# Optimization experiments

Hardware: AMD Instinct MI355X
Metric: run time of the kernel (lower is better)

## Reference

```python
import jax, jax.numpy as jnp
import numpy as np

B = 4096        # batch size (graphs)
NPB = 64        # nodes per graph
G = 8           # max_groups; first G nodes of each graph are group super-nodes
D = 128         # node_dim
GD = 128        # global_dim
H = 64          # hidden_dim
NEG = jnp.float32(-1e9)


def setup_inputs() -> dict:
    key = jax.random.key(0)
    k = jax.random.split(key, 5)
    node_features = jax.random.normal(k[0], (B * NPB, D), dtype=jnp.float32)
    global_features = jax.random.normal(k[1], (B, GD), dtype=jnp.float32)
    # nodes sorted by graph: graph b owns rows [b*NPB, (b+1)*NPB)
    batch = jnp.repeat(jnp.arange(B, dtype=jnp.int64), NPB)
    local_id = jnp.tile(jnp.arange(NPB), B)
    group_mask_nodes = local_id < G            # exactly G group nodes per graph, in order
    dock_mask = jax.random.bernoulli(k[2], 0.7, (B, G, G))
    W1 = jax.random.normal(k[3], (GD + 2 * D, H), dtype=jnp.float32) * 0.05
    b1 = jnp.zeros((H,), dtype=jnp.float32)
    W2 = jax.random.normal(k[4], (H, 1), dtype=jnp.float32) * 0.05
    b2 = jnp.zeros((1,), dtype=jnp.float32)
    return {
        "node_features": node_features,
        "global_features": global_features,
        "group_mask_nodes": group_mask_nodes,
        "batch": batch,
        "dock_mask": dock_mask,
        "W1": W1, "b1": b1, "W2": W2, "b2": b2,
    }


def reference(node_features, global_features, group_mask_nodes, batch, dock_mask, W1, b1, W2, b2):
    bsz = global_features.shape[0]
    g = dock_mask.shape[1]
    d = node_features.shape[-1]
    # Gather group super-nodes. Rows are sorted by graph with exactly g group
    # nodes per graph, so a static-size nonzero reshapes to [B, G, D] preserving
    # the row order the torch loop relies on.
    idx = jnp.nonzero(group_mask_nodes, size=bsz * g)[0]
    group_nodes = node_features[idx].reshape(bsz, g, d)           # [B,G,D]
    # Build all (i,j) pair features: [global_b, g_i, g_j] -> [B,G,G,GD+2D]
    glob = jnp.broadcast_to(global_features[:, None, None, :], (bsz, g, g, global_features.shape[-1]))
    gi = jnp.broadcast_to(group_nodes[:, :, None, :], (bsz, g, g, d))
    gj = jnp.broadcast_to(group_nodes[:, None, :, :], (bsz, g, g, d))
    inp = jnp.concatenate([glob, gi, gj], axis=-1)
    # Tiny 2-layer MLP scorer, fully batched over all pairs.
    h = jax.nn.relu(jnp.einsum('bijf,fh->bijh', inp, W1) + b1)
    scores = jnp.einsum('bijh,ho->bijo', h, W2)[..., 0] + b2[0]   # [B,G,G]
    offdiag = ~jnp.eye(g, dtype=bool)
    logits = jnp.where(offdiag[None, :, :], scores, NEG)
    logits = jnp.where(dock_mask, logits, NEG)
    return logits.reshape(bsz, g * g)
```

## Files before the change

kernel.cpp:

```cpp
#include <hip/hip_runtime.h>
#include <hip/hip_bf16.h>

#define NEGV (-1e9f)

typedef __attribute__((ext_vector_type(8))) short short8;
typedef __attribute__((ext_vector_type(4))) float f32x4;

#define MFMA16(a, b, c) __builtin_amdgcn_mfma_f32_16x16x32_bf16(a, b, c, 0, 0, 0)

__device__ __forceinline__ unsigned short f2bf(float x) {
    union { __hip_bfloat16 h; unsigned short u; } c;
    c.h = __float2bfloat16(x);
    return c.u;
}

__device__ __forceinline__ short8 pack2(f32x4 a, f32x4 b) {
    short8 r;
    r[0] = (short)f2bf(a[0]); r[1] = (short)f2bf(a[1]);
    r[2] = (short)f2bf(a[2]); r[3] = (short)f2bf(a[3]);
    r[4] = (short)f2bf(b[0]); r[5] = (short)f2bf(b[1]);
    r[6] = (short)f2bf(b[2]); r[7] = (short)f2bf(b[3]);
    return r;
}

__device__ __forceinline__ short8 pack8(const float* v) {
    short8 r;
#pragma unroll
    for (int i = 0; i < 8; ++i) r[i] = (short)f2bf(v[i]);
    return r;
}

__global__ __launch_bounds__(256, 4) void dock_main(
    const float* __restrict__ nodes,
    const float* __restrict__ glob,
    const int*   __restrict__ dock,
    const float* __restrict__ W1,
    const float* __restrict__ b1,
    const float* __restrict__ W2,
    const float* __restrict__ b2,
    float* __restrict__ out)
{
    __shared__ __align__(16) unsigned char smem[18048];
    unsigned char* gA  = smem;
    unsigned char* gGl = smem + 8192;
    float* sPQ = (float*)smem;
    float* sA  = (float*)(smem + 16896);

    const int t    = threadIdx.x;
    const int lane = t & 63;
    const int w    = __builtin_amdgcn_readfirstlane(t >> 6);
    const int b0   = blockIdx.x * 4;
    const int lr   = lane & 15, lg = lane >> 4;

    short8 bq0f[4], bq1f[4], bgf[4];
    {
        const int n0 = w * 32 + lr;
        const int n1 = n0 + 16;
        const int ng = w * 16 + lr;
        const float* Wp0 = (n0 < 64) ? W1 + 128 * 64 + n0 : W1 + 256 * 64 + (n0 - 64);
        const float* Wp1 = (n1 < 64) ? W1 + 128 * 64 + n1 : W1 + 256 * 64 + (n1 - 64);
        const float* Wpg = W1 + ng;
#pragma unroll
        for (int kt = 0; kt < 4; ++kt) {
            float v0[8], v1[8], vg[8];
#pragma unroll
            for (int i = 0; i < 8; ++i) {
                const int k = kt * 32 + lg * 8 + i;
                v0[i] = Wp0[k * 64];
                v1[i] = Wp1[k * 64];
                vg[i] = Wpg[k * 64];
            }
            bq0f[kt] = pack8(v0);
            bq1f[kt] = pack8(v1);
            bgf[kt]  = pack8(vg);
        }
    }

    {
        int r = t >> 3, c0 = (t & 7) * 16;
        const f32x4* s4 = (const f32x4*)(nodes + ((size_t)(b0 + (r >> 3)) * 64 + (r & 7)) * 128 + c0);
        f32x4 f0 = s4[0], f1 = s4[1], f2 = s4[2], f3 = s4[3];
        int u0 = c0 >> 3;
        *(short8*)(gA + r * 256 + ((u0 ^ (r & 7)) << 4))       = pack2(f0, f1);
        *(short8*)(gA + r * 256 + (((u0 + 1) ^ (r & 7)) << 4)) = pack2(f2, f3);
    }
    {
        int r = t >> 4, c0 = (t & 15) * 8;
        short8 v = (short8)0;
        if (r < 4) {
            const f32x4* s4 = (const f32x4*)(glob + (size_t)(b0 + r) * 128 + c0);
            v = pack2(s4[0], s4[1]);
        }
        *(short8*)(gGl + r * 256 + (((c0 >> 3) ^ (r & 7)) << 4)) = v;
    }
    __syncthreads();

    f32x4 acc00 = (f32x4)0.f, acc01 = (f32x4)0.f;
    f32x4 acc10 = (f32x4)0.f, acc11 = (f32x4)0.f;
    f32x4 accA  = (f32x4)0.f;
#pragma unroll
    for (int kt = 0; kt < 4; ++kt) {
        const int sw = ((kt * 4 + lg) ^ (lr & 7)) << 4;
        short8 aG0 = *(const short8*)(gA + lr * 256 + sw);
        short8 aG1 = *(const short8*)(gA + (16 + lr) * 256 + sw);
        short8 aGl = *(const short8*)(gGl + lr * 256 + sw);
        acc00 = MFMA16(aG0, bq0f[kt], acc00);
        acc01 = MFMA16(aG0, bq1f[kt], acc01);
        acc10 = MFMA16(aG1, bq0f[kt], acc10);
        acc11 = MFMA16(aG1, bq1f[kt], acc11);
        accA  = MFMA16(aGl, bgf[kt],  accA);
    }
    __syncthreads();

#pragma unroll
    for (int r = 0; r < 4; ++r) {
        sPQ[(lg * 4 + r) * 132      + (w * 32 + lr)]      = acc00[r];
        sPQ[(lg * 4 + r) * 132      + (w * 32 + 16 + lr)] = acc01[r];
        sPQ[(16 + lg * 4 + r) * 132 + (w * 32 + lr)]      = acc10[r];
        sPQ[(16 + lg * 4 + r) * 132 + (w * 32 + 16 + lr)] = acc11[r];
    }
    if (lg == 0) {
#pragma unroll
        for (int r = 0; r < 4; ++r)
            sA[r * 68 + w * 16 + lr] = accA[r];
    }
    __syncthreads();

    const int i = lane >> 3, j = lane & 7;
    const float* aRow = sA + w * 68;
    const float* pRow = sPQ + (w * 8 + i) * 132;
    const float* qRow = sPQ + (w * 8 + j) * 132 + 64;

    float s = 0.f;
#pragma unroll
    for (int kk = 0; kk < 64; kk += 4) {
        f32x4 a4 = *(const f32x4*)(aRow + kk);
        f32x4 p4 = *(const f32x4*)(pRow + kk);
        f32x4 q4 = *(const f32x4*)(qRow + kk);
        f32x4 bb = *(const f32x4*)(b1 + kk);
        f32x4 w4 = *(const f32x4*)(W2 + kk);
#pragma unroll
        for (int u = 0; u < 4; ++u) {
            float h = a4[u] + p4[u] + q4[u] + bb[u];
            h = fmaxf(h, 0.f);
            s = fmaf(h, w4[u], s);
        }
    }
    s += b2[0];

    const int idx = (b0 + w) * 64 + lane;
    out[idx] = ((i != j) && (dock[idx] != 0)) ? s : NEGV;
}

extern "C" void kernel_launch(void* const* d_in, const int* in_sizes, int n_in,
                              void* d_out, int out_size, void* d_ws, size_t ws_size,
                              hipStream_t stream) {
    const float* nodes = (const float*)d_in[0];
    const float* glob  = (const float*)d_in[1];
    const int*   dock  = (const int*)d_in[4];
    const float* W1    = (const float*)d_in[5];
    const float* b1    = (const float*)d_in[6];
    const float* W2    = (const float*)d_in[7];
    const float* b2    = (const float*)d_in[8];
    float* out = (float*)d_out;

    const int B = in_sizes[1] / 128;
    dock_main<<<dim3(B / 4), dim3(256), 0, stream>>>(
        nodes, glob, dock, W1, b1, W2, b2, out);
}
```

Measured before the change: 14.93 us.

## Pre-pack W1 into bf16 MFMA fragments in a prep kernel

Measured after the change: 15.64 us. 1.05x slower.

```diff
diff --git a/kernel.cpp b/kernel.cpp
--- a/kernel.cpp
+++ b/kernel.cpp
@@ -23,28 +23,39 @@
     return r;
 }
 
-__device__ __forceinline__ short8 pack8(const float* v) {
-    short8 r;
-#pragma unroll
-    for (int i = 0; i < 8; ++i) r[i] = (short)f2bf(v[i]);
-    return r;
+__global__ void dock_prep(const float* __restrict__ W1, unsigned short* __restrict__ ws16) {
+    const int o = blockIdx.x * 256 + threadIdx.x;
+    const int frag = o >> 9;
+    const int lane = (o >> 3) & 63;
+    const int i    = o & 7;
+    const int w = frag / 12, rem = frag % 12, mat = rem >> 2, kt = rem & 3;
+    const int lr = lane & 15, lg = lane >> 4;
+    const int k = kt * 32 + lg * 8 + i;
+    float v;
+    if (mat == 2) {
+        v = W1[k * 64 + (w * 16 + lr)];
+    } else {
+        const int n = w * 32 + lr + (mat == 1 ? 16 : 0);
+        v = (n < 64) ? W1[(128 + k) * 64 + n] : W1[(256 + k) * 64 + (n - 64)];
+    }
+    ws16[o] = f2bf(v);
 }
 
 __global__ __launch_bounds__(256, 4) void dock_main(
     const float* __restrict__ nodes,
     const float* __restrict__ glob,
     const int*   __restrict__ dock,
-    const float* __restrict__ W1,
     const float* __restrict__ b1,
+    const float* __restrict__ b2,
     const float* __restrict__ W2,
-    const float* __restrict__ b2,
+    const unsigned short* __restrict__ ws16,
     float* __restrict__ out)
 {
-    __shared__ __align__(16) unsigned char smem[18048];
+    __shared__ __align__(16) unsigned char smem[30464];
     unsigned char* gA  = smem;
     unsigned char* gGl = smem + 8192;
-    float* sPQ = (float*)smem;
-    float* sA  = (float*)(smem + 16896);
+    float* sPQ = (float*)(smem + 12288);
+    float* sA  = (float*)(smem + 12288 + 16896);
 
     const int t    = threadIdx.x;
     const int lane = t & 63;
@@ -52,29 +63,15 @@
     const int b0   = blockIdx.x * 4;
     const int lr   = lane & 15, lg = lane >> 4;
 
-    short8 bq0f[4], bq1f[4], bgf[4];
-    {
-        const int n0 = w * 32 + lr;
-        const int n1 = n0 + 16;
-        const int ng = w * 16 + lr;
-        const float* Wp0 = (n0 < 64) ? W1 + 128 * 64 + n0 : W1 + 256 * 64 + (n0 - 64);
-        const float* Wp1 = (n1 < 64) ? W1 + 128 * 64 + n1 : W1 + 256 * 64 + (n1 - 64);
-        const float* Wpg = W1 + ng;
+    const int idx = (b0 + w) * 64 + lane;
+    const int dmask = dock[idx];
+    const float b1v = b1[w * 16 + lr];
+    const float b2v = b2[0];
+
+    short8 wf[12];
 #pragma unroll
-        for (int kt = 0; kt < 4; ++kt) {
-            float v0[8], v1[8], vg[8];
-#pragma unroll
-            for (int i = 0; i < 8; ++i) {
-                const int k = kt * 32 + lg * 8 + i;
-                v0[i] = Wp0[k * 64];
-                v1[i] = Wp1[k * 64];
-                vg[i] = Wpg[k * 64];
-            }
-            bq0f[kt] = pack8(v0);
-            bq1f[kt] = pack8(v1);
-            bgf[kt]  = pack8(vg);
-        }
-    }
+    for (int f = 0; f < 12; ++f)
+        wf[f] = *(const short8*)(ws16 + (size_t)(w * 12 + f) * 512 + lane * 8);
 
     {
         int r = t >> 3, c0 = (t & 7) * 16;
@@ -104,13 +101,12 @@
         short8 aG0 = *(const short8*)(gA + lr * 256 + sw);
         short8 aG1 = *(const short8*)(gA + (16 + lr) * 256 + sw);
         short8 aGl = *(const short8*)(gGl + lr * 256 + sw);
-        acc00 = MFMA16(aG0, bq0f[kt], acc00);
-        acc01 = MFMA16(aG0, bq1f[kt], acc01);
-        acc10 = MFMA16(aG1, bq0f[kt], acc10);
-        acc11 = MFMA16(aG1, bq1f[kt], acc11);
-        accA  = MFMA16(aGl, bgf[kt],  accA);
+        acc00 = MFMA16(aG0, wf[kt],     acc00);
+        acc01 = MFMA16(aG0, wf[4 + kt], acc01);
+        acc10 = MFMA16(aG1, wf[kt],     acc10);
+        acc11 = MFMA16(aG1, wf[4 + kt], acc11);
+        accA  = MFMA16(aGl, wf[8 + kt], accA);
     }
-    __syncthreads();
 
 #pragma unroll
     for (int r = 0; r < 4; ++r) {
@@ -122,7 +118,7 @@
     if (lg == 0) {
 #pragma unroll
         for (int r = 0; r < 4; ++r)
-            sA[r * 68 + w * 16 + lr] = accA[r];
+            sA[r * 68 + w * 16 + lr] = accA[r] + b1v;
     }
     __syncthreads();
 
@@ -137,19 +133,17 @@
         f32x4 a4 = *(const f32x4*)(aRow + kk);
         f32x4 p4 = *(const f32x4*)(pRow + kk);
         f32x4 q4 = *(const f32x4*)(qRow + kk);
-        f32x4 bb = *(const f32x4*)(b1 + kk);
         f32x4 w4 = *(const f32x4*)(W2 + kk);
 #pragma unroll
         for (int u = 0; u < 4; ++u) {
-            float h = a4[u] + p4[u] + q4[u] + bb[u];
+            float h = a4[u] + p4[u] + q4[u];
             h = fmaxf(h, 0.f);
             s = fmaf(h, w4[u], s);
         }
     }
-    s += b2[0];
+    s += b2v;
 
-    const int idx = (b0 + w) * 64 + lane;
-    out[idx] = ((i != j) && (dock[idx] != 0)) ? s : NEGV;
+    out[idx] = ((i != j) && (dmask != 0)) ? s : NEGV;
 }
 
 extern "C" void kernel_launch(void* const* d_in, const int* in_sizes, int n_in,
@@ -165,6 +159,9 @@
     float* out = (float*)d_out;
 
     const int B = in_sizes[1] / 128;
+    unsigned short* ws16 = (unsigned short*)d_ws;
+
+    dock_prep<<<dim3(96), dim3(256), 0, stream>>>(W1, ws16);
     dock_main<<<dim3(B / 4), dim3(256), 0, stream>>>(
-        nodes, glob, dock, W1, b1, W2, b2, out);
+        nodes, glob, dock, b1, b2, W2, ws16, out);
 }
```

## Load MFMA operands directly from global memory, skipping LDS staging

Applied to the files above, without the earlier changes.

Result: slower. 18.92 us (+26.7%).

```diff
diff --git a/kernel.cpp b/kernel.cpp
--- a/kernel.cpp
+++ b/kernel.cpp
@@ -36,15 +36,12 @@
     const int*   __restrict__ dock,
     const float* __restrict__ W1,
     const float* __restrict__ b1,
+    const float* __restrict__ b2,
     const float* __restrict__ W2,
-    const float* __restrict__ b2,
     float* __restrict__ out)
 {
-    __shared__ __align__(16) unsigned char smem[18048];
-    unsigned char* gA  = smem;
-    unsigned char* gGl = smem + 8192;
-    float* sPQ = (float*)smem;
-    float* sA  = (float*)(smem + 16896);
+    __shared__ float sPQ[32][132];
+    __shared__ float sA[4][68];
 
     const int t    = threadIdx.x;
     const int lane = t & 63;
@@ -52,84 +49,78 @@
     const int b0   = blockIdx.x * 4;
     const int lr   = lane & 15, lg = lane >> 4;
 
-    short8 bq0f[4], bq1f[4], bgf[4];
-    {
-        const int n0 = w * 32 + lr;
-        const int n1 = n0 + 16;
-        const int ng = w * 16 + lr;
-        const float* Wp0 = (n0 < 64) ? W1 + 128 * 64 + n0 : W1 + 256 * 64 + (n0 - 64);
-        const float* Wp1 = (n1 < 64) ? W1 + 128 * 64 + n1 : W1 + 256 * 64 + (n1 - 64);
-        const float* Wpg = W1 + ng;
-#pragma unroll
-        for (int kt = 0; kt < 4; ++kt) {
-            float v0[8], v1[8], vg[8];
-#pragma unroll
-            for (int i = 0; i < 8; ++i) {
-                const int k = kt * 32 + lg * 8 + i;
-                v0[i] = Wp0[k * 64];
-                v1[i] = Wp1[k * 64];
-                vg[i] = Wpg[k * 64];
-            }
-            bq0f[kt] = pack8(v0);
-            bq1f[kt] = pack8(v1);
-            bgf[kt]  = pack8(vg);
-        }
-    }
+    const int idx = (b0 + w) * 64 + lane;
+    const int dmask = dock[idx];
+    const float b1v = b1[w * 16 + lr];
+    const float b2v = b2[0];
 
-    {
-        int r = t >> 3, c0 = (t & 7) * 16;
-        const f32x4* s4 = (const f32x4*)(nodes + ((size_t)(b0 + (r >> 3)) * 64 + (r & 7)) * 128 + c0);
-        f32x4 f0 = s4[0], f1 = s4[1], f2 = s4[2], f3 = s4[3];
-        int u0 = c0 >> 3;
-        *(short8*)(gA + r * 256 + ((u0 ^ (r & 7)) << 4))       = pack2(f0, f1);
-        *(short8*)(gA + r * 256 + (((u0 + 1) ^ (r & 7)) << 4)) = pack2(f2, f3);
-    }
-    {
-        int r = t >> 4, c0 = (t & 15) * 8;
-        short8 v = (short8)0;
-        if (r < 4) {
-            const f32x4* s4 = (const f32x4*)(glob + (size_t)(b0 + r) * 128 + c0);
-            v = pack2(s4[0], s4[1]);
-        }
-        *(short8*)(gGl + r * 256 + (((c0 >> 3) ^ (r & 7)) << 4)) = v;
-    }
-    __syncthreads();
+    const float* pG0 = nodes + ((size_t)(b0 + (lr >> 3)) * 64 + (lr & 7)) * 128 + lg * 8;
+    const float* pG1 = nodes + ((size_t)(b0 + 2 + (lr >> 3)) * 64 + (lr & 7)) * 128 + lg * 8;
+    const float* pGl = glob + (size_t)(b0 + lr) * 128 + lg * 8;
+
+    const int n0 = w * 32 + lr;
+    const int n1 = n0 + 16;
+    const float* Wp0 = (n0 < 64) ? W1 + 128 * 64 + n0 : W1 + 256 * 64 + (n0 - 64);
+    const float* Wp1 = (n1 < 64) ? W1 + 128 * 64 + n1 : W1 + 256 * 64 + (n1 - 64);
+    const float* Wpg = W1 + (w * 16 + lr);
 
     f32x4 acc00 = (f32x4)0.f, acc01 = (f32x4)0.f;
     f32x4 acc10 = (f32x4)0.f, acc11 = (f32x4)0.f;
     f32x4 accA  = (f32x4)0.f;
+
 #pragma unroll
     for (int kt = 0; kt < 4; ++kt) {
-        const int sw = ((kt * 4 + lg) ^ (lr & 7)) << 4;
-        short8 aG0 = *(const short8*)(gA + lr * 256 + sw);
-        short8 aG1 = *(const short8*)(gA + (16 + lr) * 256 + sw);
-        short8 aGl = *(const short8*)(gGl + lr * 256 + sw);
-        acc00 = MFMA16(aG0, bq0f[kt], acc00);
-        acc01 = MFMA16(aG0, bq1f[kt], acc01);
-        acc10 = MFMA16(aG1, bq0f[kt], acc10);
-        acc11 = MFMA16(aG1, bq1f[kt], acc11);
-        accA  = MFMA16(aGl, bgf[kt],  accA);
+        float v0[8], v1[8], vg[8];
+#pragma unroll
+        for (int i = 0; i < 8; ++i) {
+            const int k = kt * 32 + lg * 8 + i;
+            v0[i] = Wp0[k * 64];
+            v1[i] = Wp1[k * 64];
+            vg[i] = Wpg[k * 64];
+        }
+        f32x4 a0l = *(const f32x4*)(pG0 + kt * 32);
+        f32x4 a0h = *(const f32x4*)(pG0 + kt * 32 + 4);
+        f32x4 a1l = *(const f32x4*)(pG1 + kt * 32);
+        f32x4 a1h = *(const f32x4*)(pG1 + kt * 32 + 4);
+        short8 aGl;
+        if (lr < 4) {
+            f32x4 gl_ = *(const f32x4*)(pGl + kt * 32);
+            f32x4 gh_ = *(const f32x4*)(pGl + kt * 32 + 4);
+            aGl = pack2(gl_, gh_);
+        } else {
+            aGl = (short8)0;
+        }
+        short8 aG0 = pack2(a0l, a0h);
+        short8 aG1 = pack2(a1l, a1h);
+        short8 bf0 = pack8(v0);
+        short8 bf1 = pack8(v1);
+        short8 bfg = pack8(vg);
+
+        acc00 = MFMA16(aG0, bf0, acc00);
+        acc01 = MFMA16(aG0, bf1, acc01);
+        acc10 = MFMA16(aG1, bf0, acc10);
+        acc11 = MFMA16(aG1, bf1, acc11);
+        accA  = MFMA16(aGl, bfg, accA);
     }
-    __syncthreads();
 
 #pragma unroll
     for (int r = 0; r < 4; ++r) {
-        sPQ[(lg * 4 + r) * 132      + (w * 32 + lr)]      = acc00[r];
-        sPQ[(lg * 4 + r) * 132      + (w * 32 + 16 + lr)] = acc01[r];
-        sPQ[(16 + lg * 4 + r) * 132 + (w * 32 + lr)]      = acc10[r];
-        sPQ[(16 + lg * 4 + r) * 132 + (w * 32 + 16 + lr)] = acc11[r];
+        sPQ[lg * 4 + r][w * 32 + lr]           = acc00[r];
+        sPQ[lg * 4 + r][w * 32 + 16 + lr]      = acc01[r];
+        sPQ[16 + lg * 4 + r][w * 32 + lr]      = acc10[r];
+        sPQ[16 + lg * 4 + r][w * 32 + 16 + lr] = acc11[r];
     }
     if (lg == 0) {
 #pragma unroll
         for (int r = 0; r < 4; ++r)
-            sA[r * 68 + w * 16 + lr] = accA[r];
+            sA[r][w * 16 + lr] = accA[r] + b1v;
     }
     __syncthreads();
 
     const int i = lane >> 3, j = lane & 7;
-    const float* aRow = sA + w * 68;
-    const float* pRow = sPQ + (w * 8 + i) * 132;
-    const float* qRow = sPQ + (w * 8 + j) * 132 + 64;
+    const float* aRow = &sA[w][0];
+    const float* pRow = &sPQ[w * 8 + i][0];
+    const float* qRow = &sPQ[w * 8 + j][64];
 
     float s = 0.f;
 #pragma unroll
@@ -137,19 +128,17 @@
         f32x4 a4 = *(const f32x4*)(aRow + kk);
         f32x4 p4 = *(const f32x4*)(pRow + kk);
         f32x4 q4 = *(const f32x4*)(qRow + kk);
-        f32x4 bb = *(const f32x4*)(b1 + kk);
         f32x4 w4 = *(const f32x4*)(W2 + kk);
 #pragma unroll
         for (int u = 0; u < 4; ++u) {
-            float h = a4[u] + p4[u] + q4[u] + bb[u];
+            float h = a4[u] + p4[u] + q4[u];
             h = fmaxf(h, 0.f);
             s = fmaf(h, w4[u], s);
         }
     }
-    s += b2[0];
+    s += b2v;
 
-    const int idx = (b0 + w) * 64 + lane;
-    out[idx] = ((i != j) && (dock[idx] != 0)) ? s : NEGV;
+    out[idx] = ((i != j) && (dmask != 0)) ? s : NEGV;
 }
 
 extern "C" void kernel_launch(void* const* d_in, const int* in_sizes, int n_in,
@@ -166,5 +155,5 @@
 
     const int B = in_sizes[1] / 128;
     dock_main<<<dim3(B / 4), dim3(256), 0, stream>>>(
-        nodes, glob, dock, W1, b1, W2, b2, out);
+        nodes, glob, dock, W1, b1, b2, W2, out);
 }
```
